# Optimization experiments

Measured on AMD Instinct MI355X. Metric: run time of the kernel, lower is better.

## Reference

```python
import jax, jax.numpy as jnp
import numpy as np

B, S, D = 2, 2048, 1024
H = 16
HD = D // H  # 64

def setup_inputs() -> dict:
    key = jax.random.key(0)
    ks = jax.random.split(key, 6)
    scale = 0.02
    x   = jax.random.normal(ks[0], (B, S, D), dtype=jnp.float32)
    Wq  = jax.random.normal(ks[1], (D, D), dtype=jnp.float32) * scale
    Wk  = jax.random.normal(ks[2], (D, D), dtype=jnp.float32) * scale
    Wv  = jax.random.normal(ks[3], (D, D), dtype=jnp.float32) * scale
    Wo  = jax.random.normal(ks[4], (D, D), dtype=jnp.float32) * scale
    bo  = jax.random.normal(ks[5], (D,), dtype=jnp.float32) * scale
    return {"x": x, "Wq": Wq, "Wk": Wk, "Wv": Wv, "Wo": Wo, "bo": bo}

def reference(x, Wq, Wk, Wv, Wo, bo):
    b, s, d = x.shape
    # QKV projections (no bias, qkv_bias=False); weights stored as [d_in, d_out]
    q = (x @ Wq).reshape(b, s, H, HD).transpose(0, 2, 1, 3)  # [b,h,s,hd]
    k = (x @ Wk).reshape(b, s, H, HD).transpose(0, 2, 1, 3)
    v = (x @ Wv).reshape(b, s, H, HD).transpose(0, 2, 1, 3)
    scores = jnp.einsum('bhqd,bhkd->bhqk', q, k)  # [b,h,s,s]
    causal = jnp.triu(jnp.ones((s, s), dtype=bool), k=1)
    scores = jnp.where(causal, -jnp.inf, scores)
    attn = jax.nn.softmax(scores / jnp.sqrt(jnp.float32(HD)), axis=-1)
    # dropout_rate = 0.0 -> identity
    ctx = jnp.einsum('bhqk,bhkd->bqhd', attn, v).reshape(b, s, d)
    return ctx @ Wo + bo
```

## Files before the change

### kernel.cpp

```cpp
#include <hip/hip_runtime.h>
#include <hip/hip_bf16.h>
#include <math.h>

#define B_ 2
#define S_ 2048
#define D_ 1024
#define H_ 16
#define HD_ 64
#define M_ (B_*S_)

typedef __attribute__((ext_vector_type(8))) short bf16x8;
typedef __attribute__((ext_vector_type(4))) float f32x4;

#define MFMA16(a,b,c) __builtin_amdgcn_mfma_f32_16x16x32_bf16(a,b,c,0,0,0)
#define INFF __builtin_inff()

static __device__ __forceinline__ unsigned short f2bf_bits(float f) {
    unsigned int u = __float_as_uint(f);
    unsigned int r = (u + 0x7fffu + ((u >> 16) & 1u)) >> 16;
    return (unsigned short)r;
}

static __device__ __forceinline__ void gload16(const unsigned short* g, unsigned short* l) {
    __builtin_amdgcn_global_load_lds(
        (const __attribute__((address_space(1))) unsigned int*)(g),
        (__attribute__((address_space(3))) unsigned int*)(l),
        16, 0, 0);
}

__global__ __launch_bounds__(256) void convert_x_kernel(
    const float* __restrict__ x, unsigned short* __restrict__ o) {
    size_t i = (size_t)blockIdx.x * 256 + threadIdx.x;
    float4 v = reinterpret_cast<const float4*>(x)[i];
    ushort4 u;
    u.x = f2bf_bits(v.x); u.y = f2bf_bits(v.y);
    u.z = f2bf_bits(v.z); u.w = f2bf_bits(v.w);
    reinterpret_cast<ushort4*>(o)[i] = u;
}

__global__ __launch_bounds__(256) void convw_kernel(
    const float* __restrict__ W0, const float* __restrict__ W1,
    const float* __restrict__ W2, const float* __restrict__ W3,
    unsigned short* __restrict__ OT) {
    __shared__ float t[32][33];
    const float* W = (blockIdx.z == 0) ? W0 : (blockIdx.z == 1) ? W1
                    : (blockIdx.z == 2) ? W2 : W3;
    unsigned short* O = OT + (size_t)blockIdx.z * D_ * D_;
    int tx = threadIdx.x & 31, ty = threadIdx.x >> 5;
    int kb = blockIdx.y * 32, nb = blockIdx.x * 32;
#pragma unroll
    for (int i = 0; i < 4; i++)
        t[ty + 8*i][tx] = W[(size_t)(kb + ty + 8*i) * D_ + nb + tx];
    __syncthreads();
#pragma unroll
    for (int i = 0; i < 4; i++) {
        int n = nb + ty + 8*i, k = kb + tx;
        O[(size_t)n * D_ + k] = f2bf_bits(t[tx][ty + 8*i]);
    }
}

template<int BN, int MODE>
__global__ __launch_bounds__(256) void gemm_gl(
    const unsigned short* __restrict__ A,
    const unsigned short* __restrict__ BT,
    void* __restrict__ outp,
    const float* __restrict__ bias)
{
    constexpr int K = 1024;
    constexpr int NF = (BN == 128) ? 4 : 2;
    __shared__ union {
        struct { unsigned short As[128][64]; unsigned short Bs[BN][64]; } g;
        unsigned short vt[(BN == 128) ? 128 : 1][136];
    } sm;
    const int m0 = blockIdx.x * 128;
    const int n0 = blockIdx.y * BN;
    const int tid = threadIdx.x, lane = tid & 63, wid = tid >> 6;
    const int wm = (wid >> 1) * 64;
    const int wn = (wid & 1) * (BN / 2);
    const int lrow = lane & 15, lk8 = lane >> 4, orow = lk8 * 4;
    f32x4 acc[4][NF] = {};

    for (int k0 = 0; k0 < K; k0 += 64) {
#pragma unroll
        for (int i = 0; i < 4; i++) {
            const int rbase = wid * 32 + i * 8;
            const int rl = rbase + (lane >> 3);
            const int sc = ((lane & 7) ^ (rl & 7)) << 3;
            gload16(A + (size_t)(m0 + rl) * K + k0 + sc, &sm.g.As[rbase][0]);
        }
#pragma unroll
        for (int i = 0; i < BN / 32; i++) {
            const int rbase = wid * (BN / 4) + i * 8;
            const int rl = rbase + (lane >> 3);
            const int sc = ((lane & 7) ^ (rl & 7)) << 3;
            gload16(BT + (size_t)(n0 + rl) * K + k0 + sc, &sm.g.Bs[rbase][0]);
        }
        __syncthreads();
#pragma unroll
        for (int ks = 0; ks < 2; ks++) {
            bf16x8 af[4], bfr[NF];
#pragma unroll
            for (int f = 0; f < 4; f++) {
                const int row = wm + f * 16 + lrow;
                const int p = (ks * 4 + lk8) ^ (row & 7);
                af[f] = *reinterpret_cast<const bf16x8*>(&sm.g.As[row][p * 8]);
            }
#pragma unroll
            for (int f = 0; f < NF; f++) {
                const int row = wn + f * 16 + lrow;
                const int p = (ks * 4 + lk8) ^ (row & 7);
                bfr[f] = *reinterpret_cast<const bf16x8*>(&sm.g.Bs[row][p * 8]);
            }
            __builtin_amdgcn_s_setprio(1);
#pragma unroll
            for (int mf = 0; mf < 4; mf++)
#pragma unroll
                for (int nf = 0; nf < NF; nf++)
                    acc[mf][nf] = MFMA16(af[mf], bfr[nf], acc[mf][nf]);
            __builtin_amdgcn_s_setprio(0);
        }
        __syncthreads();
    }

    if (MODE == 0) {
        const int which = n0 >> 10;
        const int nl0 = n0 & 1023;
        unsigned short* obase = (unsigned short*)outp + (size_t)which * 4194304;
        const float scale = (which == 0) ? 0.125f : 1.0f;
        if (which < 2) {
#pragma unroll
            for (int mf = 0; mf < 4; mf++)
#pragma unroll
                for (int nf = 0; nf < NF; nf++)
#pragma unroll
                    for (int r = 0; r < 4; r++) {
                        int m = m0 + wm + mf*16 + orow + r;
                        int n = nl0 + wn + nf*16 + lrow;
                        int b = m >> 11, s = m & 2047;
                        int h = n >> 6, hd = n & 63;
                        obase[(((size_t)(b*16 + h) * 2048 + s) << 6) + hd]
                            = f2bf_bits(acc[mf][nf][r] * scale);
                    }
        } else {
#pragma unroll
            for (int mf = 0; mf < 4; mf++)
#pragma unroll
                for (int nf = 0; nf < NF; nf++)
#pragma unroll
                    for (int r = 0; r < 4; r++)
                        sm.vt[wn + nf*16 + lrow][wm + mf*16 + orow + r] =
                            f2bf_bits(acc[mf][nf][r]);
            __syncthreads();
            const int n = tid >> 1, c0 = (tid & 1) * 64;
            const int ng = nl0 + n, h = ng >> 6, hd = ng & 63;
            const int b = m0 >> 11, sbase = (m0 & 2047) + c0;
            unsigned short* dst = obase +
                (((size_t)(b * 16 + h) * 64 + hd) * 2048 + sbase);
#pragma unroll
            for (int j = 0; j < 64; j += 8)
                *reinterpret_cast<bf16x8*>(dst + j) =
                    *reinterpret_cast<const bf16x8*>(&sm.vt[n][c0 + j]);
        }
    } else {
        float* o = (float*)outp;
#pragma unroll
        for (int mf = 0; mf < 4; mf++)
#pragma unroll
            for (int nf = 0; nf < NF; nf++)
#pragma unroll
                for (int r = 0; r < 4; r++) {
                    int m = m0 + wm + mf*16 + orow + r;
                    int n = n0 + wn + nf*16 + lrow;
                    o[(size_t)m * 1024 + n] = acc[mf][nf][r] + bias[n];
                }
    }
}

__global__ __launch_bounds__(256) void attn_kernel(
    const unsigned short* __restrict__ Q,
    const unsigned short* __restrict__ Kb,
    const unsigned short* __restrict__ VT,
    unsigned short* __restrict__ ctx)
{
    __shared__ unsigned short Ks[2][64][64];
    __shared__ unsigned short Vs[2][64][64];
    __shared__ unsigned short Pl[4][16][72];
    const int fid = blockIdx.x;
    const int xcd = fid & 7, t = fid >> 3;
    const int bh = xcd | ((t & 3) << 3);
    const int qt = 31 - (t >> 2);
    const int lane = threadIdx.x & 63, wid = threadIdx.x >> 6;
    const int lrow = lane & 15, lk8 = lane >> 4, orow = lk8 * 4;
    const unsigned short* Qp = Q  + (size_t)bh * (S_ * 64);
    const unsigned short* Kp = Kb + (size_t)bh * (S_ * 64);
    const unsigned short* Vp = VT + (size_t)bh * (64 * S_);
    const int b = bh >> 4, h = bh & 15;
    const int q0 = qt * 64 + wid * 16;
    const int nb = qt + 1;

    auto stage = [&](int buf, int kv0) {
#pragma unroll
        for (int i = 0; i < 2; i++) {
            const int rbase = wid * 16 + 8 * i;
            const int rl = rbase + (lane >> 3);
            const int sc = (((lane & 7) ^ (rl & 7)) << 3);
            gload16(Kp + (size_t)(kv0 + rl) * 64 + sc, &Ks[buf][rbase][0]);
            gload16(Vp + (size_t)rl * S_ + kv0 + sc, &Vs[buf][rbase][0]);
        }
    };

    stage(0, 0);

    bf16x8 qf[2];
#pragma unroll
    for (int kt = 0; kt < 2; kt++)
        qf[kt] = *reinterpret_cast<const bf16x8*>(
            Qp + (size_t)(q0 + lrow) * 64 + kt*32 + lk8*8);

    f32x4 acc[4] = {};
    float lr = 0.f;

    __syncthreads();

#pragma unroll 1
    for (int kvb = 0; kvb < nb; kvb++) {
        const int cur = kvb & 1;
        if (kvb + 1 < nb) stage(cur ^ 1, (kvb + 1) * 64);

        f32x4 sacc[4] = {};
        __builtin_amdgcn_s_setprio(1);
#pragma unroll
        for (int kt = 0; kt < 2; kt++)
#pragma unroll
            for (int nf = 0; nf < 4; nf++) {
                const int row = nf * 16 + lrow;
                const int g = ((kt << 2) | lk8) ^ (row & 7);
                bf16x8 kf = *reinterpret_cast<const bf16x8*>(&Ks[cur][row][g << 3]);
                sacc[nf] = MFMA16(kf, qf[kt], sacc[nf]);
            }
        __builtin_amdgcn_s_setprio(0);
        if (kvb == qt) {
#pragma unroll
            for (int nf = 0; nf < 4; nf++)
#pragma unroll
                for (int r = 0; r < 4; r++)
                    if (nf*16 + orow + r > wid*16 + lrow) sacc[nf][r] = -INFF;
        }
#pragma unroll
        for (int nf = 0; nf < 4; nf++)
#pragma unroll
            for (int r = 0; r < 4; r++) {
                float p = __expf(sacc[nf][r]);
                sacc[nf][r] = p;
                lr += p;
            }
#pragma unroll
        for (int nf = 0; nf < 4; nf++) {
            uint2 w;
            w.x = (unsigned)f2bf_bits(sacc[nf][0]) | ((unsigned)f2bf_bits(sacc[nf][1]) << 16);
            w.y = (unsigned)f2bf_bits(sacc[nf][2]) | ((unsigned)f2bf_bits(sacc[nf][3]) << 16);
            *reinterpret_cast<uint2*>(&Pl[wid][lrow][nf*16 + orow]) = w;
        }
        bf16x8 pf[2];
#pragma unroll
        for (int kt = 0; kt < 2; kt++)
            pf[kt] = *reinterpret_cast<const bf16x8*>(&Pl[wid][lrow][kt*32 + lk8*8]);
        __builtin_amdgcn_s_setprio(1);
#pragma unroll
        for (int kt = 0; kt < 2; kt++)
#pragma unroll
            for (int nf = 0; nf < 4; nf++) {
                const int row = nf * 16 + lrow;
                const int g = ((kt << 2) | lk8) ^ (row & 7);
                bf16x8 vf = *reinterpret_cast<const bf16x8*>(&Vs[cur][row][g << 3]);
                acc[nf] = MFMA16(pf[kt], vf, acc[nf]);
            }
        __builtin_amdgcn_s_setprio(0);
        __syncthreads();
    }

    lr += __shfl_xor(lr, 16);
    lr += __shfl_xor(lr, 32);
    const float inv = 1.0f / lr;
#pragma unroll
    for (int r = 0; r < 4; r++) {
        const float linv = __shfl(inv, (lane & 48) + orow + r);
#pragma unroll
        for (int nf = 0; nf < 4; nf++) {
            int s = q0 + orow + r;
            int col = h * 64 + nf * 16 + lrow;
            ctx[((size_t)(b * S_ + s)) * D_ + col] = f2bf_bits(acc[nf][r] * linv);
        }
    }
}

extern "C" void kernel_launch(void* const* d_in, const int* in_sizes, int n_in,
                              void* d_out, int out_size, void* d_ws, size_t ws_size,
                              hipStream_t stream) {
    const float* x  = (const float*)d_in[0];
    const float* Wq = (const float*)d_in[1];
    const float* Wk = (const float*)d_in[2];
    const float* Wv = (const float*)d_in[3];
    const float* Wo = (const float*)d_in[4];
    const float* bo = (const float*)d_in[5];
    float* out = (float*)d_out;

    char* ws = (char*)d_ws;
    unsigned short* xb  = (unsigned short*)(ws);
    unsigned short* WT  = (unsigned short*)(ws + 8388608);
    unsigned short* QKV = (unsigned short*)(ws + 16777216);
    unsigned short* ctx = (unsigned short*)(ws + 41943040);

    unsigned short* Qb  = QKV;
    unsigned short* Kb  = QKV + 4194304;
    unsigned short* VTb = QKV + 8388608;

    convert_x_kernel<<<dim3(4096), dim3(256), 0, stream>>>(x, xb);
    convw_kernel<<<dim3(32, 32, 4), dim3(256), 0, stream>>>(Wq, Wk, Wv, Wo, WT);

    gemm_gl<128, 0><<<dim3(32, 24), dim3(256), 0, stream>>>(
        xb, WT, (void*)QKV, (const float*)nullptr);

    attn_kernel<<<dim3(1024), dim3(256), 0, stream>>>(Qb, Kb, VTb, ctx);

    gemm_gl<64, 1><<<dim3(32, 16), dim3(256), 0, stream>>>(
        ctx, WT + 3145728, (void*)out, bo);
}
```

Baseline: 112.6 us.

## Replace QKV GEMM with 256x256 double-buffered 8-wave pipelined kernel

Adds a dedicated QKV projection GEMM that uses 256x256 tiles, 512 threads, and double-buffered LDS. Each K step is split into four phases that interleave the async global-to-LDS loads for the next step with MFMA work on the current quadrant, using partial vmcnt waits and barriers. Larger tiles are meant to raise arithmetic intensity and hide load latency, at the cost of only 192 blocks and higher LDS and register pressure. The generic GEMM keeps only the output-projection epilogue.

After: 134.9 us. 19.8% more time.

```diff
diff --git a/kernel.cpp b/kernel.cpp
--- a/kernel.cpp
+++ b/kernel.cpp
@@ -27,6 +27,13 @@
         (__attribute__((address_space(3))) unsigned int*)(l),
         16, 0, 0);
 }
+
+#define PH_END do { \
+    asm volatile("s_waitcnt vmcnt(4)" ::: "memory"); \
+    __builtin_amdgcn_sched_barrier(0); \
+    __builtin_amdgcn_s_barrier(); \
+    __builtin_amdgcn_sched_barrier(0); \
+} while (0)
 
 __global__ __launch_bounds__(256) void convert_x_kernel(
     const float* __restrict__ x, unsigned short* __restrict__ o) {
@@ -59,6 +66,151 @@
     }
 }
 
+__global__ __launch_bounds__(512, 2) void gemm_qkv256(
+    const unsigned short* __restrict__ A,
+    const unsigned short* __restrict__ BT,
+    unsigned short* __restrict__ outp)
+{
+    constexpr int K = 1024;
+    __shared__ union {
+        struct { unsigned short A[2][2][128*64]; unsigned short B[2][2][128*64]; } s;
+        unsigned short vt[256][136];
+    } sm;
+    const int m0 = blockIdx.x * 256;
+    const int n0 = blockIdx.y * 256;
+    const int tid = threadIdx.x, lane = tid & 63, wid = tid >> 6;
+    const int lrow = lane & 15, lk8 = lane >> 4, orow = lk8 * 4;
+    const int wmo = (wid >> 2) * 64;
+    const int wno = (wid & 3) * 32;
+    const int srow = lane >> 3;
+    const int sgr  = lane & 7;
+
+    f32x4 acc[8][4] = {};
+    bf16x8 af[4][2], bf[2][2];
+
+    auto stageA = [&](int par, int mh, int k0) {
+#pragma unroll
+        for (int j = 0; j < 2; j++) {
+            const int rb = wid * 8 + j * 64;
+            const int rl = rb + srow;
+            const int sc = (sgr ^ (rl & 7)) << 3;
+            gload16(A + (size_t)(m0 + mh * 128 + rl) * K + k0 + sc,
+                    &sm.s.A[par][mh][rb * 64]);
+        }
+    };
+    auto stageB = [&](int par, int nh, int k0) {
+#pragma unroll
+        for (int j = 0; j < 2; j++) {
+            const int rb = wid * 8 + j * 64;
+            const int rl = rb + srow;
+            const int sc = (sgr ^ (rl & 7)) << 3;
+            gload16(BT + (size_t)(n0 + nh * 128 + rl) * K + k0 + sc,
+                    &sm.s.B[par][nh][rb * 64]);
+        }
+    };
+    auto lda = [&](int par, int qm) {
+        const unsigned short* ap = &sm.s.A[par][qm][0];
+#pragma unroll
+        for (int f = 0; f < 4; f++)
+#pragma unroll
+            for (int ks = 0; ks < 2; ks++) {
+                const int rr = wmo + f * 16 + lrow;
+                af[f][ks] = *reinterpret_cast<const bf16x8*>(
+                    &ap[rr * 64 + (((ks << 2) | lk8) ^ (rr & 7)) * 8]);
+            }
+    };
+    auto ldb = [&](int par, int qn) {
+        const unsigned short* bp = &sm.s.B[par][qn][0];
+#pragma unroll
+        for (int g = 0; g < 2; g++)
+#pragma unroll
+            for (int ks = 0; ks < 2; ks++) {
+                const int rr = wno + g * 16 + lrow;
+                bf[g][ks] = *reinterpret_cast<const bf16x8*>(
+                    &bp[rr * 64 + (((ks << 2) | lk8) ^ (rr & 7)) * 8]);
+            }
+    };
+    auto mma = [&](int qm, int qn) {
+        __builtin_amdgcn_s_setprio(1);
+#pragma unroll
+        for (int f = 0; f < 4; f++)
+#pragma unroll
+            for (int g = 0; g < 2; g++)
+#pragma unroll
+                for (int ks = 0; ks < 2; ks++)
+                    acc[qm*4+f][qn*2+g] =
+                        MFMA16(af[f][ks], bf[g][ks], acc[qm*4+f][qn*2+g]);
+        __builtin_amdgcn_s_setprio(0);
+    };
+
+    stageA(0, 0, 0); stageB(0, 0, 0); stageB(0, 1, 0); stageA(0, 1, 0);
+    PH_END;
+
+#pragma unroll 1
+    for (int t = 0; t < 16; t++) {
+        const int par = t & 1, pn = par ^ 1;
+        const int kn = (t < 15) ? (t + 1) * 64 : 0;
+        lda(par, 0); ldb(par, 0);  stageA(pn, 0, kn);  mma(0, 0);  PH_END;
+        ldb(par, 1);               stageB(pn, 0, kn);  mma(0, 1);  PH_END;
+        lda(par, 1);               stageB(pn, 1, kn);  mma(1, 1);  PH_END;
+        ldb(par, 0);               stageA(pn, 1, kn);  mma(1, 0);  PH_END;
+    }
+
+    asm volatile("s_waitcnt vmcnt(0)" ::: "memory");
+    __builtin_amdgcn_sched_barrier(0);
+    __builtin_amdgcn_s_barrier();
+
+    const int which = n0 >> 10;
+    const int nl0 = n0 & 1023;
+    const int bq = m0 >> 11;
+    unsigned short* obase = outp + (size_t)which * 4194304;
+
+    if (which < 2) {
+        const float scale = (which == 0) ? 0.125f : 1.0f;
+#pragma unroll
+        for (int fi = 0; fi < 8; fi++)
+#pragma unroll
+            for (int g = 0; g < 4; g++)
+#pragma unroll
+                for (int r = 0; r < 4; r++) {
+                    int m = m0 + (fi >> 2) * 128 + wmo + (fi & 3) * 16 + orow + r;
+                    int n = nl0 + (g >> 1) * 128 + wno + (g & 1) * 16 + lrow;
+                    int s = m & 2047;
+                    obase[(((size_t)(bq * 16 + (n >> 6)) * 2048 + s) << 6) + (n & 63)]
+                        = f2bf_bits(acc[fi][g][r] * scale);
+                }
+    } else {
+#pragma unroll 1
+        for (int qm = 0; qm < 2; qm++) {
+#pragma unroll
+            for (int f = 0; f < 4; f++)
+#pragma unroll
+                for (int g = 0; g < 4; g++) {
+                    const int ml = wmo + f * 16 + orow;
+                    const int nc = (g >> 1) * 128 + wno + (g & 1) * 16 + lrow;
+                    uint2 w;
+                    w.x = (unsigned)f2bf_bits(acc[qm*4+f][g][0])
+                        | ((unsigned)f2bf_bits(acc[qm*4+f][g][1]) << 16);
+                    w.y = (unsigned)f2bf_bits(acc[qm*4+f][g][2])
+                        | ((unsigned)f2bf_bits(acc[qm*4+f][g][3]) << 16);
+                    *reinterpret_cast<uint2*>(&sm.vt[nc][ml]) = w;
+                }
+            __syncthreads();
+            {
+                const int row = tid >> 1, c0 = (tid & 1) * 64;
+                unsigned short* dst = obase +
+                    ((size_t)(bq * 1024) + nl0 + row) * 2048 +
+                    (m0 & 2047) + qm * 128 + c0;
+#pragma unroll
+                for (int j = 0; j < 64; j += 8)
+                    *reinterpret_cast<bf16x8*>(dst + j) =
+                        *reinterpret_cast<const bf16x8*>(&sm.vt[row][c0 + j]);
+            }
+            __syncthreads();
+        }
+    }
+}
+
 template<int BN, int MODE>
 __global__ __launch_bounds__(256) void gemm_gl(
     const unsigned short* __restrict__ A,
@@ -68,10 +220,7 @@
 {
     constexpr int K = 1024;
     constexpr int NF = (BN == 128) ? 4 : 2;
-    __shared__ union {
-        struct { unsigned short As[128][64]; unsigned short Bs[BN][64]; } g;
-        unsigned short vt[(BN == 128) ? 128 : 1][136];
-    } sm;
+    __shared__ struct { unsigned short As[128][64]; unsigned short Bs[BN][64]; } sm;
     const int m0 = blockIdx.x * 128;
     const int n0 = blockIdx.y * BN;
     const int tid = threadIdx.x, lane = tid & 63, wid = tid >> 6;
@@ -86,14 +235,14 @@
             const int rbase = wid * 32 + i * 8;
             const int rl = rbase + (lane >> 3);
             const int sc = ((lane & 7) ^ (rl & 7)) << 3;
-            gload16(A + (size_t)(m0 + rl) * K + k0 + sc, &sm.g.As[rbase][0]);
+            gload16(A + (size_t)(m0 + rl) * K + k0 + sc, &sm.As[rbase][0]);
         }
 #pragma unroll
         for (int i = 0; i < BN / 32; i++) {
             const int rbase = wid * (BN / 4) + i * 8;
             const int rl = rbase + (lane >> 3);
             const int sc = ((lane & 7) ^ (rl & 7)) << 3;
-            gload16(BT + (size_t)(n0 + rl) * K + k0 + sc, &sm.g.Bs[rbase][0]);
+            gload16(BT + (size_t)(n0 + rl) * K + k0 + sc, &sm.Bs[rbase][0]);
         }
         __syncthreads();
 #pragma unroll
@@ -103,13 +252,13 @@
             for (int f = 0; f < 4; f++) {
                 const int row = wm + f * 16 + lrow;
                 const int p = (ks * 4 + lk8) ^ (row & 7);
-                af[f] = *reinterpret_cast<const bf16x8*>(&sm.g.As[row][p * 8]);
+                af[f] = *reinterpret_cast<const bf16x8*>(&sm.As[row][p * 8]);
             }
 #pragma unroll
             for (int f = 0; f < NF; f++) {
                 const int row = wn + f * 16 + lrow;
                 const int p = (ks * 4 + lk8) ^ (row & 7);
-                bfr[f] = *reinterpret_cast<const bf16x8*>(&sm.g.Bs[row][p * 8]);
+                bfr[f] = *reinterpret_cast<const bf16x8*>(&sm.Bs[row][p * 8]);
             }
             __builtin_amdgcn_s_setprio(1);
 #pragma unroll
@@ -122,58 +271,17 @@
         __syncthreads();
     }
 
-    if (MODE == 0) {
-        const int which = n0 >> 10;
-        const int nl0 = n0 & 1023;
-        unsigned short* obase = (unsigned short*)outp + (size_t)which * 4194304;
-        const float scale = (which == 0) ? 0.125f : 1.0f;
-        if (which < 2) {
-#pragma unroll
-            for (int mf = 0; mf < 4; mf++)
-#pragma unroll
-                for (int nf = 0; nf < NF; nf++)
-#pragma unroll
-                    for (int r = 0; r < 4; r++) {
-                        int m = m0 + wm + mf*16 + orow + r;
-                        int n = nl0 + wn + nf*16 + lrow;
-                        int b = m >> 11, s = m & 2047;
-                        int h = n >> 6, hd = n & 63;
-                        obase[(((size_t)(b*16 + h) * 2048 + s) << 6) + hd]
-                            = f2bf_bits(acc[mf][nf][r] * scale);
-                    }
-        } else {
-#pragma unroll
-            for (int mf = 0; mf < 4; mf++)
-#pragma unroll
-                for (int nf = 0; nf < NF; nf++)
-#pragma unroll
-                    for (int r = 0; r < 4; r++)
-                        sm.vt[wn + nf*16 + lrow][wm + mf*16 + orow + r] =
-                            f2bf_bits(acc[mf][nf][r]);
-            __syncthreads();
-            const int n = tid >> 1, c0 = (tid & 1) * 64;
-            const int ng = nl0 + n, h = ng >> 6, hd = ng & 63;
-            const int b = m0 >> 11, sbase = (m0 & 2047) + c0;
-            unsigned short* dst = obase +
-                (((size_t)(b * 16 + h) * 64 + hd) * 2048 + sbase);
-#pragma unroll
-            for (int j = 0; j < 64; j += 8)
-                *reinterpret_cast<bf16x8*>(dst + j) =
-                    *reinterpret_cast<const bf16x8*>(&sm.vt[n][c0 + j]);
-        }
-    } else {
-        float* o = (float*)outp;
-#pragma unroll
-        for (int mf = 0; mf < 4; mf++)
-#pragma unroll
-            for (int nf = 0; nf < NF; nf++)
-#pragma unroll
-                for (int r = 0; r < 4; r++) {
-                    int m = m0 + wm + mf*16 + orow + r;
-                    int n = n0 + wn + nf*16 + lrow;
-                    o[(size_t)m * 1024 + n] = acc[mf][nf][r] + bias[n];
-                }
-    }
+    float* o = (float*)outp;
+#pragma unroll
+    for (int mf = 0; mf < 4; mf++)
+#pragma unroll
+        for (int nf = 0; nf < NF; nf++)
+#pragma unroll
+            for (int r = 0; r < 4; r++) {
+                int m = m0 + wm + mf*16 + orow + r;
+                int n = n0 + wn + nf*16 + lrow;
+                o[(size_t)m * 1024 + n] = acc[mf][nf][r] + bias[n];
+            }
 }
 
 __global__ __launch_bounds__(256) void attn_kernel(
@@ -318,8 +426,7 @@
     convert_x_kernel<<<dim3(4096), dim3(256), 0, stream>>>(x, xb);
     convw_kernel<<<dim3(32, 32, 4), dim3(256), 0, stream>>>(Wq, Wk, Wv, Wo, WT);
 
-    gemm_gl<128, 0><<<dim3(32, 24), dim3(256), 0, stream>>>(
-        xb, WT, (void*)QKV, (const float*)nullptr);
+    gemm_qkv256<<<dim3(16, 12), dim3(512), 0, stream>>>(xb, WT, QKV);
 
     attn_kernel<<<dim3(1024), dim3(256), 0, stream>>>(Qb, Kb, VTb, ctx);
 
```
